# Optimization experiments

Hardware: AMD Instinct MI355X
Metric: run time of the kernel (lower is better)

## Reference

```python
import jax, jax.numpy as jnp
import numpy as np

BINS = 10

def setup_inputs() -> dict:
    key = jax.random.key(0)
    k1, k2 = jax.random.split(key)
    shape = (8, 80000, 80)
    inputs = jax.random.normal(k1, shape, dtype=jnp.float32)
    # binary 0/1 float labels
    targets = jax.random.randint(k2, shape, 0, 2).astype(jnp.float32)
    return {"inputs": inputs, "targets": targets}

def reference(inputs, targets):
    bins = BINS
    tot = inputs.size  # static python int
    p = jax.nn.sigmoid(inputs)
    g = jnp.abs(p - targets)  # gradient norm proxy, in [0, 1]
    # bin index: edges are i/bins, i=0..bins (last edge +1e-6 so g==1 falls in last bin)
    idx = jnp.clip(jnp.floor(g * bins).astype(jnp.int32), 0, bins - 1)
    # single-pass histogram over all elements
    counts = jax.ops.segment_sum(
        jnp.ones((tot,), dtype=jnp.float32), idx.reshape(-1), num_segments=bins
    )
    n = jnp.sum(counts > 0).astype(inputs.dtype)  # number of non-empty bins
    bin_w = jnp.where(counts > 0, tot / jnp.maximum(counts, 1.0), 0.0)
    weights = bin_w[idx] / jnp.maximum(n, 1.0)
    # weights are constant w.r.t. inputs in the torch code (num_in_bin via .item())
    weights = jax.lax.stop_gradient(weights)
    # stable binary_cross_entropy_with_logits, elementwise ('none' reduction)
    bce = jnp.maximum(inputs, 0.0) - inputs * targets + jnp.log1p(jnp.exp(-jnp.abs(inputs)))
    return (weights * bce) / tot
```

## Files before the change

### kernel.cpp

```cpp
#include <hip/hip_runtime.h>
#include <math.h>

#define NBINS 10
#define TOT_F 51200000.0f
#define NREPL 64
#define REPL_STRIDE 16

typedef float f32x4 __attribute__((ext_vector_type(4)));

__device__ __forceinline__ float np_expf(float x) {
    const float LOG2E = 1.442695040f;
    float z = x * LOG2E;
    float q = __builtin_rintf(z);
    float r = __builtin_fmaf(q, -0.693359375f, x);
    r = __builtin_fmaf(q, 2.12194440e-4f, r);
    float rr = r * r;
    float p = 1.9875691500e-4f;
    p = __builtin_fmaf(p, r, 1.3981999507e-3f);
    p = __builtin_fmaf(p, r, 8.3334519073e-3f);
    p = __builtin_fmaf(p, r, 4.1665795894e-2f);
    p = __builtin_fmaf(p, r, 1.6666665459e-1f);
    p = __builtin_fmaf(p, r, 5.0000001201e-1f);
    p = __builtin_fmaf(p, rr, r);
    p = p + 1.0f;
    return ldexpf(p, (int)q);
}

__device__ __forceinline__ int bin_index(float x, float t) {
    float e = np_expf(-x);
    float p = 1.0f / (1.0f + e);
    float g = fabsf(p - t);
    float d = g * 10.0f;
    int idx = (int)d;
    return idx > (NBINS - 1) ? (NBINS - 1) : idx;
}

__global__ void ghm_init_k(unsigned int* __restrict__ counts) {
    int i = threadIdx.x;
    if (i < NREPL * REPL_STRIDE) counts[i] = 0u;
}

__device__ __forceinline__ void acc4(unsigned int c[NBINS], float4 x, float4 t) {
    int i0 = bin_index(x.x, t.x);
    int i1 = bin_index(x.y, t.y);
    int i2 = bin_index(x.z, t.z);
    int i3 = bin_index(x.w, t.w);
#pragma unroll
    for (int b = 0; b < NBINS; ++b)
        c[b] += (unsigned int)(i0 == b) + (unsigned int)(i1 == b) +
                (unsigned int)(i2 == b) + (unsigned int)(i3 == b);
}

__global__ void __launch_bounds__(256, 4)
ghm_hist_k(const float4* __restrict__ x4,
           const float4* __restrict__ t4,
           const float*  __restrict__ x1,
           const float*  __restrict__ t1,
           unsigned int* __restrict__ counts,
           int n4, int n) {
    unsigned int c[NBINS];
#pragma unroll
    for (int i = 0; i < NBINS; ++i) c[i] = 0u;

    int gsz = gridDim.x * blockDim.x;
    int i = blockIdx.x * blockDim.x + threadIdx.x;
    int lim = n4 - 3 * gsz;
    for (; i < lim; i += 4 * gsz) {
        float4 xa = x4[i];
        float4 xb = x4[i + gsz];
        float4 xc = x4[i + 2 * gsz];
        float4 xd = x4[i + 3 * gsz];
        float4 ta = t4[i];
        float4 tb = t4[i + gsz];
        float4 tc = t4[i + 2 * gsz];
        float4 td = t4[i + 3 * gsz];
        acc4(c, xa, ta); acc4(c, xb, tb); acc4(c, xc, tc); acc4(c, xd, td);
    }
    for (; i < n4; i += gsz) {
        float4 x = x4[i];
        float4 t = t4[i];
        acc4(c, x, t);
    }
    int tail = n - n4 * 4;
    if (blockIdx.x == 0 && (int)threadIdx.x < tail) {
        int k = n4 * 4 + threadIdx.x;
        int ix = bin_index(x1[k], t1[k]);
#pragma unroll
        for (int b = 0; b < NBINS; ++b) c[b] += (unsigned int)(ix == b);
    }

    __shared__ unsigned int ls[4][NBINS];
    int lane = threadIdx.x & 63;
    int wv = threadIdx.x >> 6;
#pragma unroll
    for (int b = 0; b < NBINS; ++b) {
        unsigned int v = c[b];
#pragma unroll
        for (int off = 32; off > 0; off >>= 1)
            v += __shfl_down(v, off, 64);
        if (lane == 0) ls[wv][b] = v;
    }
    __syncthreads();
    if (threadIdx.x < NBINS) {
        unsigned int s = ls[0][threadIdx.x] + ls[1][threadIdx.x] +
                         ls[2][threadIdx.x] + ls[3][threadIdx.x];
        if (s) atomicAdd(&counts[(blockIdx.x & 63) * REPL_STRIDE + threadIdx.x], s);
    }
}

__global__ void ghm_weights_k(const unsigned int* __restrict__ counts,
                              float* __restrict__ W) {
    __shared__ unsigned int tot[NBINS];
    if (threadIdx.x < NBINS) tot[threadIdx.x] = 0u;
    __syncthreads();
    if (threadIdx.x < NREPL * NBINS) {
        int r = threadIdx.x / NBINS;
        int b = threadIdx.x % NBINS;
        unsigned int v = counts[r * REPL_STRIDE + b];
        if (v) atomicAdd(&tot[b], v);
    }
    __syncthreads();
    if (threadIdx.x == 0) {
        int n = 0;
        for (int i = 0; i < NBINS; ++i) n += (tot[i] > 0u);
        float nf = fmaxf((float)n, 1.0f);
        for (int i = 0; i < NBINS; ++i) {
            float cf = (float)tot[i];
            float bw = (tot[i] > 0u) ? (TOT_F / fmaxf(cf, 1.0f)) : 0.0f;
            W[i] = (bw / nf) / TOT_F;
        }
    }
}

__device__ __forceinline__ float ghm_elem(float x, float t,
                                          const float* __restrict__ sW) {
    int idx = bin_index(x, t);
    float bce = fmaxf(x, 0.0f) - x * t + log1pf(__expf(-fabsf(x)));
    return sW[idx] * bce;
}

__device__ __forceinline__ float4 elem4(float4 x, float4 t,
                                        const float* __restrict__ sW) {
    float4 o;
    o.x = ghm_elem(x.x, t.x, sW);
    o.y = ghm_elem(x.y, t.y, sW);
    o.z = ghm_elem(x.z, t.z, sW);
    o.w = ghm_elem(x.w, t.w, sW);
    return o;
}

__device__ __forceinline__ void nt_store(float4* p, float4 v) {
    __builtin_nontemporal_store(*(f32x4*)&v, (f32x4*)p);
}

__global__ void __launch_bounds__(256, 4)
ghm_main_k(const float4* __restrict__ x4,
           const float4* __restrict__ t4,
           const float*  __restrict__ x1,
           const float*  __restrict__ t1,
           const float*  __restrict__ W,
           float4* __restrict__ o4,
           float*  __restrict__ o1,
           int n4, int n) {
    __shared__ float sW[NBINS];
    if (threadIdx.x < NBINS) sW[threadIdx.x] = W[threadIdx.x];
    __syncthreads();

    int gsz = gridDim.x * blockDim.x;
    int i = blockIdx.x * blockDim.x + threadIdx.x;
    int lim = n4 - 3 * gsz;
    for (; i < lim; i += 4 * gsz) {
        float4 xa = x4[i];
        float4 xb = x4[i + gsz];
        float4 xc = x4[i + 2 * gsz];
        float4 xd = x4[i + 3 * gsz];
        float4 ta = t4[i];
        float4 tb = t4[i + gsz];
        float4 tc = t4[i + 2 * gsz];
        float4 td = t4[i + 3 * gsz];
        nt_store(&o4[i],           elem4(xa, ta, sW));
        nt_store(&o4[i + gsz],     elem4(xb, tb, sW));
        nt_store(&o4[i + 2 * gsz], elem4(xc, tc, sW));
        nt_store(&o4[i + 3 * gsz], elem4(xd, td, sW));
    }
    for (; i < n4; i += gsz) {
        float4 x = x4[i];
        float4 t = t4[i];
        nt_store(&o4[i], elem4(x, t, sW));
    }
    int tail = n - n4 * 4;
    if (blockIdx.x == 0 && (int)threadIdx.x < tail) {
        int k = n4 * 4 + threadIdx.x;
        o1[k] = ghm_elem(x1[k], t1[k], sW);
    }
}

extern "C" void kernel_launch(void* const* d_in, const int* in_sizes, int n_in,
                              void* d_out, int out_size, void* d_ws, size_t ws_size,
                              hipStream_t stream) {
    const float* x = (const float*)d_in[0];
    const float* t = (const float*)d_in[1];
    float* out = (float*)d_out;
    int n  = in_sizes[0];
    int n4 = n >> 2;

    unsigned int* counts = (unsigned int*)d_ws;
    float* W = (float*)((char*)d_ws + NREPL * REPL_STRIDE * 4);

    const int threads = 256;
    const int blocks  = 2048;

    ghm_init_k<<<1, 1024, 0, stream>>>(counts);
    ghm_hist_k<<<blocks, threads, 0, stream>>>(
        (const float4*)x, (const float4*)t, x, t, counts, n4, n);
    ghm_weights_k<<<1, 1024, 0, stream>>>(counts, W);
    ghm_main_k<<<blocks, threads, 0, stream>>>(
        (const float4*)x, (const float4*)t, x, t, W,
        (float4*)out, out, n4, n);
}
```

Measured before the change: 609.4 us.

## Cache per-element bin indices as bytes between histogram and apply passes

The first pass now computes bin indices once and stores them as packed bytes in the workspace, so the apply pass skips recomputing the sigmoid. Histogram counting uses 6-bit fields packed into one 64-bit register with periodic drains. Per-block counts go to an array instead of atomics, which also drops the init kernel. Binning uses the fast reciprocal, with an exact-division fallback near bin edges. The apply pass walks the data in reverse order to pick up cache hits left by pass one. Costs are an extra 51 MB write and read of indices and a dependency on workspace size; the old path is kept as a fallback.

```diff
diff --git a/kernel.cpp b/kernel.cpp
--- a/kernel.cpp
+++ b/kernel.cpp
@@ -3,6 +3,7 @@
 
 #define NBINS 10
 #define TOT_F 51200000.0f
+#define BMARG 2e-5f
 #define NREPL 64
 #define REPL_STRIDE 16
 
@@ -26,7 +27,7 @@
     return ldexpf(p, (int)q);
 }
 
-__device__ __forceinline__ int bin_index(float x, float t) {
+__device__ __forceinline__ int bin_index_ref(float x, float t) {
     float e = np_expf(-x);
     float p = 1.0f / (1.0f + e);
     float g = fabsf(p - t);
@@ -35,16 +36,207 @@
     return idx > (NBINS - 1) ? (NBINS - 1) : idx;
 }
 
+__device__ __forceinline__ unsigned bin4(float4 x, float4 t,
+                                         unsigned long long& a64) {
+    float e0 = np_expf(-x.x), e1 = np_expf(-x.y);
+    float e2 = np_expf(-x.z), e3 = np_expf(-x.w);
+    float s0 = 1.0f + e0, s1 = 1.0f + e1, s2 = 1.0f + e2, s3 = 1.0f + e3;
+    float d0 = fabsf(__builtin_amdgcn_rcpf(s0) - t.x) * 10.0f;
+    float d1 = fabsf(__builtin_amdgcn_rcpf(s1) - t.y) * 10.0f;
+    float d2 = fabsf(__builtin_amdgcn_rcpf(s2) - t.z) * 10.0f;
+    float d3 = fabsf(__builtin_amdgcn_rcpf(s3) - t.w) * 10.0f;
+    int i0 = (int)d0, i1 = (int)d1, i2 = (int)d2, i3 = (int)d3;
+    float f0 = d0 - (float)i0, f1 = d1 - (float)i1;
+    float f2 = d2 - (float)i2, f3 = d3 - (float)i3;
+    float fmn = fminf(fminf(f0, f1), fminf(f2, f3));
+    float fmx = fmaxf(fmaxf(f0, f1), fmaxf(f2, f3));
+    if (fmn < BMARG || fmx > 1.0f - BMARG) {
+        d0 = fabsf(1.0f / s0 - t.x) * 10.0f; i0 = (int)d0;
+        d1 = fabsf(1.0f / s1 - t.y) * 10.0f; i1 = (int)d1;
+        d2 = fabsf(1.0f / s2 - t.z) * 10.0f; i2 = (int)d2;
+        d3 = fabsf(1.0f / s3 - t.w) * 10.0f; i3 = (int)d3;
+    }
+    i0 = i0 > 9 ? 9 : i0; i1 = i1 > 9 ? 9 : i1;
+    i2 = i2 > 9 ? 9 : i2; i3 = i3 > 9 ? 9 : i3;
+    a64 += (1ULL << (i0 * 6)) + (1ULL << (i1 * 6)) +
+           (1ULL << (i2 * 6)) + (1ULL << (i3 * 6));
+    return (unsigned)i0 | ((unsigned)i1 << 8) |
+           ((unsigned)i2 << 16) | ((unsigned)i3 << 24);
+}
+
+__device__ __forceinline__ int bin1(float x, float t) {
+    float e = np_expf(-x);
+    float s = 1.0f + e;
+    float d = fabsf(__builtin_amdgcn_rcpf(s) - t) * 10.0f;
+    int di = (int)d;
+    float f = d - (float)di;
+    if (f < BMARG || f > 1.0f - BMARG) {
+        d = fabsf(1.0f / s - t) * 10.0f;
+        di = (int)d;
+    }
+    return di > 9 ? 9 : di;
+}
+
+__device__ __forceinline__ float bce1(float x, float t) {
+    float e = __expf(-fabsf(x));
+    return fmaxf(x, 0.0f) - x * t + __logf(1.0f + e);
+}
+
+__device__ __forceinline__ void nt_store(float4* p, float4 v) {
+    __builtin_nontemporal_store(*(f32x4*)&v, (f32x4*)p);
+}
+
+#define DRAIN64()                                                        \
+    do {                                                                 \
+        _Pragma("unroll")                                                \
+        for (int b = 0; b < NBINS; ++b)                                  \
+            c[b] += (unsigned)((a64 >> (6 * b)) & 63ULL);                \
+        a64 = 0ULL;                                                      \
+    } while (0)
+
+__global__ void __launch_bounds__(256, 4)
+ghm_pass1_k(const float4* __restrict__ x4, const float4* __restrict__ t4,
+            const float* __restrict__ x1, const float* __restrict__ t1,
+            unsigned int* __restrict__ idxw,
+            unsigned int* __restrict__ bcounts,
+            int n4, int n, int nblocks) {
+    unsigned c[NBINS];
+#pragma unroll
+    for (int i = 0; i < NBINS; ++i) c[i] = 0u;
+    unsigned long long a64 = 0ULL;
+    int since = 0;
+
+    int gsz = gridDim.x * blockDim.x;
+    int tid = blockIdx.x * blockDim.x + threadIdx.x;
+    int nChunk = n4 >> 2;
+    for (int ch = tid; ch < nChunk; ch += gsz) {
+        int j = ch << 2;
+        float4 xa = x4[j],     xb = x4[j + 1],  xc = x4[j + 2],  xd = x4[j + 3];
+        float4 ta = t4[j],     tb = t4[j + 1],  tc = t4[j + 2],  td = t4[j + 3];
+        uint4 P;
+        P.x = bin4(xa, ta, a64);
+        P.y = bin4(xb, tb, a64);
+        P.z = bin4(xc, tc, a64);
+        P.w = bin4(xd, td, a64);
+        ((uint4*)idxw)[ch] = P;
+        if (++since == 3) { since = 0; DRAIN64(); }
+    }
+    DRAIN64();
+
+    if (blockIdx.x == 0) {
+        for (int j = (nChunk << 2) + (int)threadIdx.x; j < n4; j += blockDim.x) {
+            float4 x = x4[j], t = t4[j];
+            idxw[j] = bin4(x, t, a64);
+        }
+        int tail = n - n4 * 4;
+        if ((int)threadIdx.x < tail) {
+            int k = n4 * 4 + threadIdx.x;
+            int ix = bin1(x1[k], t1[k]);
+            ((unsigned char*)idxw)[k] = (unsigned char)ix;
+            a64 += 1ULL << (ix * 6);
+        }
+        DRAIN64();
+    }
+
+    __shared__ unsigned ls[4][NBINS];
+    int lane = threadIdx.x & 63;
+    int wv = threadIdx.x >> 6;
+#pragma unroll
+    for (int b = 0; b < NBINS; ++b) {
+        unsigned v = c[b];
+#pragma unroll
+        for (int off = 32; off > 0; off >>= 1)
+            v += __shfl_down(v, off, 64);
+        if (lane == 0) ls[wv][b] = v;
+    }
+    __syncthreads();
+    if (threadIdx.x < NBINS) {
+        unsigned s = ls[0][threadIdx.x] + ls[1][threadIdx.x] +
+                     ls[2][threadIdx.x] + ls[3][threadIdx.x];
+        bcounts[threadIdx.x * nblocks + blockIdx.x] = s;
+    }
+}
+
+__global__ void ghm_wreduce_k(const unsigned int* __restrict__ bc,
+                              float* __restrict__ W, int nblocks) {
+    __shared__ unsigned tot[NBINS];
+    int b = threadIdx.x >> 6, r = threadIdx.x & 63;
+    unsigned s = 0;
+    for (int j = r; j < nblocks; j += 64) s += bc[b * nblocks + j];
+#pragma unroll
+    for (int off = 32; off > 0; off >>= 1) s += __shfl_down(s, off, 64);
+    if (r == 0) tot[b] = s;
+    __syncthreads();
+    if (threadIdx.x == 0) {
+        int nn = 0;
+        for (int i = 0; i < NBINS; ++i) nn += (tot[i] > 0u);
+        float nf = fmaxf((float)nn, 1.0f);
+        for (int i = 0; i < NBINS; ++i) {
+            float cf = (float)tot[i];
+            float bw = (tot[i] > 0u) ? (TOT_F / fmaxf(cf, 1.0f)) : 0.0f;
+            W[i] = (bw / nf) / TOT_F;
+        }
+    }
+}
+
+__device__ __forceinline__ float4 apply4(float4 x, float4 t, unsigned pk,
+                                         const float* __restrict__ sW) {
+    float4 o;
+    o.x = sW[pk & 255u]         * bce1(x.x, t.x);
+    o.y = sW[(pk >> 8) & 255u]  * bce1(x.y, t.y);
+    o.z = sW[(pk >> 16) & 255u] * bce1(x.z, t.z);
+    o.w = sW[pk >> 24]          * bce1(x.w, t.w);
+    return o;
+}
+
+__global__ void __launch_bounds__(256, 4)
+ghm_apply_k(const float4* __restrict__ x4, const float4* __restrict__ t4,
+            const float* __restrict__ x1, const float* __restrict__ t1,
+            const unsigned int* __restrict__ idxw,
+            const float* __restrict__ W,
+            float4* __restrict__ o4, float* __restrict__ o1,
+            int n4, int n) {
+    __shared__ float sW[NBINS];
+    if (threadIdx.x < NBINS) sW[threadIdx.x] = W[threadIdx.x];
+    __syncthreads();
+
+    int gsz = gridDim.x * blockDim.x;
+    int tid = blockIdx.x * blockDim.x + threadIdx.x;
+    int nChunk = n4 >> 2;
+    for (int ch = tid; ch < nChunk; ch += gsz) {
+        int cr = nChunk - 1 - ch;
+        int j = cr << 2;
+        uint4 P = ((const uint4*)idxw)[cr];
+        float4 xa = x4[j],     xb = x4[j + 1],  xc = x4[j + 2],  xd = x4[j + 3];
+        float4 ta = t4[j],     tb = t4[j + 1],  tc = t4[j + 2],  td = t4[j + 3];
+        nt_store(&o4[j],     apply4(xa, ta, P.x, sW));
+        nt_store(&o4[j + 1], apply4(xb, tb, P.y, sW));
+        nt_store(&o4[j + 2], apply4(xc, tc, P.z, sW));
+        nt_store(&o4[j + 3], apply4(xd, td, P.w, sW));
+    }
+    if (blockIdx.x == 0) {
+        for (int j = (nChunk << 2) + (int)threadIdx.x; j < n4; j += blockDim.x) {
+            float4 x = x4[j], t = t4[j];
+            nt_store(&o4[j], apply4(x, t, idxw[j], sW));
+        }
+        int tail = n - n4 * 4;
+        if ((int)threadIdx.x < tail) {
+            int k = n4 * 4 + threadIdx.x;
+            o1[k] = sW[((const unsigned char*)idxw)[k]] * bce1(x1[k], t1[k]);
+        }
+    }
+}
+
 __global__ void ghm_init_k(unsigned int* __restrict__ counts) {
     int i = threadIdx.x;
     if (i < NREPL * REPL_STRIDE) counts[i] = 0u;
 }
 
 __device__ __forceinline__ void acc4(unsigned int c[NBINS], float4 x, float4 t) {
-    int i0 = bin_index(x.x, t.x);
-    int i1 = bin_index(x.y, t.y);
-    int i2 = bin_index(x.z, t.z);
-    int i3 = bin_index(x.w, t.w);
+    int i0 = bin_index_ref(x.x, t.x);
+    int i1 = bin_index_ref(x.y, t.y);
+    int i2 = bin_index_ref(x.z, t.z);
+    int i3 = bin_index_ref(x.w, t.w);
 #pragma unroll
     for (int b = 0; b < NBINS; ++b)
         c[b] += (unsigned int)(i0 == b) + (unsigned int)(i1 == b) +
@@ -52,52 +244,35 @@
 }
 
 __global__ void __launch_bounds__(256, 4)
-ghm_hist_k(const float4* __restrict__ x4,
-           const float4* __restrict__ t4,
-           const float*  __restrict__ x1,
-           const float*  __restrict__ t1,
-           unsigned int* __restrict__ counts,
-           int n4, int n) {
+ghm_hist_k(const float4* __restrict__ x4, const float4* __restrict__ t4,
+           const float* __restrict__ x1, const float* __restrict__ t1,
+           unsigned int* __restrict__ counts, int n4, int n) {
     unsigned int c[NBINS];
 #pragma unroll
     for (int i = 0; i < NBINS; ++i) c[i] = 0u;
-
     int gsz = gridDim.x * blockDim.x;
     int i = blockIdx.x * blockDim.x + threadIdx.x;
     int lim = n4 - 3 * gsz;
     for (; i < lim; i += 4 * gsz) {
-        float4 xa = x4[i];
-        float4 xb = x4[i + gsz];
-        float4 xc = x4[i + 2 * gsz];
-        float4 xd = x4[i + 3 * gsz];
-        float4 ta = t4[i];
-        float4 tb = t4[i + gsz];
-        float4 tc = t4[i + 2 * gsz];
-        float4 td = t4[i + 3 * gsz];
+        float4 xa = x4[i], xb = x4[i + gsz], xc = x4[i + 2 * gsz], xd = x4[i + 3 * gsz];
+        float4 ta = t4[i], tb = t4[i + gsz], tc = t4[i + 2 * gsz], td = t4[i + 3 * gsz];
         acc4(c, xa, ta); acc4(c, xb, tb); acc4(c, xc, tc); acc4(c, xd, td);
     }
-    for (; i < n4; i += gsz) {
-        float4 x = x4[i];
-        float4 t = t4[i];
-        acc4(c, x, t);
-    }
+    for (; i < n4; i += gsz) { float4 x = x4[i], t = t4[i]; acc4(c, x, t); }
     int tail = n - n4 * 4;
     if (blockIdx.x == 0 && (int)threadIdx.x < tail) {
         int k = n4 * 4 + threadIdx.x;
-        int ix = bin_index(x1[k], t1[k]);
+        int ix = bin_index_ref(x1[k], t1[k]);
 #pragma unroll
         for (int b = 0; b < NBINS; ++b) c[b] += (unsigned int)(ix == b);
     }
-
     __shared__ unsigned int ls[4][NBINS];
-    int lane = threadIdx.x & 63;
-    int wv = threadIdx.x >> 6;
+    int lane = threadIdx.x & 63, wv = threadIdx.x >> 6;
 #pragma unroll
     for (int b = 0; b < NBINS; ++b) {
         unsigned int v = c[b];
 #pragma unroll
-        for (int off = 32; off > 0; off >>= 1)
-            v += __shfl_down(v, off, 64);
+        for (int off = 32; off > 0; off >>= 1) v += __shfl_down(v, off, 64);
         if (lane == 0) ls[wv][b] = v;
     }
     __syncthreads();
@@ -114,16 +289,15 @@
     if (threadIdx.x < NBINS) tot[threadIdx.x] = 0u;
     __syncthreads();
     if (threadIdx.x < NREPL * NBINS) {
-        int r = threadIdx.x / NBINS;
-        int b = threadIdx.x % NBINS;
+        int r = threadIdx.x / NBINS, b = threadIdx.x % NBINS;
         unsigned int v = counts[r * REPL_STRIDE + b];
         if (v) atomicAdd(&tot[b], v);
     }
     __syncthreads();
     if (threadIdx.x == 0) {
-        int n = 0;
-        for (int i = 0; i < NBINS; ++i) n += (tot[i] > 0u);
-        float nf = fmaxf((float)n, 1.0f);
+        int nn = 0;
+        for (int i = 0; i < NBINS; ++i) nn += (tot[i] > 0u);
+        float nf = fmaxf((float)nn, 1.0f);
         for (int i = 0; i < NBINS; ++i) {
             float cf = (float)tot[i];
             float bw = (tot[i] > 0u) ? (TOT_F / fmaxf(cf, 1.0f)) : 0.0f;
@@ -132,66 +306,29 @@
     }
 }
 
-__device__ __forceinline__ float ghm_elem(float x, float t,
-                                          const float* __restrict__ sW) {
-    int idx = bin_index(x, t);
-    float bce = fmaxf(x, 0.0f) - x * t + log1pf(__expf(-fabsf(x)));
-    return sW[idx] * bce;
-}
-
-__device__ __forceinline__ float4 elem4(float4 x, float4 t,
-                                        const float* __restrict__ sW) {
-    float4 o;
-    o.x = ghm_elem(x.x, t.x, sW);
-    o.y = ghm_elem(x.y, t.y, sW);
-    o.z = ghm_elem(x.z, t.z, sW);
-    o.w = ghm_elem(x.w, t.w, sW);
-    return o;
-}
-
-__device__ __forceinline__ void nt_store(float4* p, float4 v) {
-    __builtin_nontemporal_store(*(f32x4*)&v, (f32x4*)p);
-}
-
 __global__ void __launch_bounds__(256, 4)
-ghm_main_k(const float4* __restrict__ x4,
-           const float4* __restrict__ t4,
-           const float*  __restrict__ x1,
-           const float*  __restrict__ t1,
-           const float*  __restrict__ W,
-           float4* __restrict__ o4,
-           float*  __restrict__ o1,
-           int n4, int n) {
+ghm_main_k(const float4* __restrict__ x4, const float4* __restrict__ t4,
+           const float* __restrict__ x1, const float* __restrict__ t1,
+           const float* __restrict__ W,
+           float4* __restrict__ o4, float* __restrict__ o1, int n4, int n) {
     __shared__ float sW[NBINS];
     if (threadIdx.x < NBINS) sW[threadIdx.x] = W[threadIdx.x];
     __syncthreads();
-
     int gsz = gridDim.x * blockDim.x;
     int i = blockIdx.x * blockDim.x + threadIdx.x;
-    int lim = n4 - 3 * gsz;
-    for (; i < lim; i += 4 * gsz) {
-        float4 xa = x4[i];
-        float4 xb = x4[i + gsz];
-        float4 xc = x4[i + 2 * gsz];
-        float4 xd = x4[i + 3 * gsz];
-        float4 ta = t4[i];
-        float4 tb = t4[i + gsz];
-        float4 tc = t4[i + 2 * gsz];
-        float4 td = t4[i + 3 * gsz];
-        nt_store(&o4[i],           elem4(xa, ta, sW));
-        nt_store(&o4[i + gsz],     elem4(xb, tb, sW));
-        nt_store(&o4[i + 2 * gsz], elem4(xc, tc, sW));
-        nt_store(&o4[i + 3 * gsz], elem4(xd, td, sW));
-    }
     for (; i < n4; i += gsz) {
-        float4 x = x4[i];
-        float4 t = t4[i];
-        nt_store(&o4[i], elem4(x, t, sW));
+        float4 x = x4[i], t = t4[i];
+        float4 o;
+        o.x = sW[bin_index_ref(x.x, t.x)] * bce1(x.x, t.x);
+        o.y = sW[bin_index_ref(x.y, t.y)] * bce1(x.y, t.y);
+        o.z = sW[bin_index_ref(x.z, t.z)] * bce1(x.z, t.z);
+        o.w = sW[bin_index_ref(x.w, t.w)] * bce1(x.w, t.w);
+        nt_store(&o4[i], o);
     }
     int tail = n - n4 * 4;
     if (blockIdx.x == 0 && (int)threadIdx.x < tail) {
         int k = n4 * 4 + threadIdx.x;
-        o1[k] = ghm_elem(x1[k], t1[k], sW);
+        o1[k] = sW[bin_index_ref(x1[k], t1[k])] * bce1(x1[k], t1[k]);
     }
 }
 
@@ -204,17 +341,35 @@
     int n  = in_sizes[0];
     int n4 = n >> 2;
 
-    unsigned int* counts = (unsigned int*)d_ws;
-    float* W = (float*)((char*)d_ws + NREPL * REPL_STRIDE * 4);
-
     const int threads = 256;
     const int blocks  = 2048;
 
-    ghm_init_k<<<1, 1024, 0, stream>>>(counts);
-    ghm_hist_k<<<blocks, threads, 0, stream>>>(
-        (const float4*)x, (const float4*)t, x, t, counts, n4, n);
-    ghm_weights_k<<<1, 1024, 0, stream>>>(counts, W);
-    ghm_main_k<<<blocks, threads, 0, stream>>>(
-        (const float4*)x, (const float4*)t, x, t, W,
-        (float4*)out, out, n4, n);
-}
+    size_t idxBytes = ((size_t)n + 15) & ~(size_t)15;
+    size_t cntOff   = idxBytes;
+    size_t cntBytes = (size_t)blocks * NBINS * sizeof(unsigned);
+    size_t wOff     = cntOff + ((cntBytes + 63) & ~(size_t)63);
+    size_t need     = wOff + 64;
+
+    if (ws_size >= need) {
+        unsigned int* idxw    = (unsigned int*)d_ws;
+        unsigned int* bcounts = (unsigned int*)((char*)d_ws + cntOff);
+        float* W              = (float*)((char*)d_ws + wOff);
+
+        ghm_pass1_k<<<blocks, threads, 0, stream>>>(
+            (const float4*)x, (const float4*)t, x, t, idxw, bcounts, n4, n, blocks);
+        ghm_wreduce_k<<<1, 640, 0, stream>>>(bcounts, W, blocks);
+        ghm_apply_k<<<blocks, threads, 0, stream>>>(
+            (const float4*)x, (const float4*)t, x, t, idxw, W,
+            (float4*)out, out, n4, n);
+    } else {
+        unsigned int* counts = (unsigned int*)d_ws;
+        float* W = (float*)((char*)d_ws + NREPL * REPL_STRIDE * 4);
+        ghm_init_k<<<1, 1024, 0, stream>>>(counts);
+        ghm_hist_k<<<blocks, threads, 0, stream>>>(
+            (const float4*)x, (const float4*)t, x, t, counts, n4, n);
+        ghm_weights_k<<<1, 1024, 0, stream>>>(counts, W);
+        ghm_main_k<<<blocks, threads, 0, stream>>>(
+            (const float4*)x, (const float4*)t, x, t, W,
+            (float4*)out, out, n4, n);
+    }
+}
```

New measurement: 796.7 us. 30.7% more time.
